# Performance work log

Hardware: AMD Instinct MI355X
Metric: run time of the kernel (lower is better)

Reference implementation:

```python
import jax, jax.numpy as jnp
import numpy as np

N = 100000   # nodes
E = 1200000  # edges
D = 64       # feature / hidden dim (heads=1)
L = 3        # num_layers
G = 64       # num graphs
SCALE = 1.0 / np.sqrt(D)


def setup_inputs() -> dict:
    key = jax.random.key(0)
    ks = jax.random.split(key, 12)
    inp = {
        "x": jax.random.normal(ks[0], (N, D), dtype=jnp.float32),
        "edge_index": jax.random.randint(ks[1], (2, E), 0, N, dtype=jnp.int64),
        "batch": jnp.sort(jax.random.randint(ks[2], (N,), 0, G, dtype=jnp.int64)),
        "Wq": jax.random.normal(ks[3], (L, D, D), dtype=jnp.float32) * 0.1,
        "bq": jax.random.normal(ks[4], (L, D), dtype=jnp.float32) * 0.1,
        "Wk": jax.random.normal(ks[5], (L, D, D), dtype=jnp.float32) * 0.1,
        "bk": jax.random.normal(ks[6], (L, D), dtype=jnp.float32) * 0.1,
        "Wv": jax.random.normal(ks[7], (L, D, D), dtype=jnp.float32) * 0.1,
        "bv": jax.random.normal(ks[8], (L, D), dtype=jnp.float32) * 0.1,
        "Ws": jax.random.normal(ks[9], (L, D, D), dtype=jnp.float32) * 0.1,
        "bs": jax.random.normal(ks[10], (L, D), dtype=jnp.float32) * 0.1,
    }
    return inp


def _transformer_conv(x, src, dst, Wq, bq, Wk, bk, Wv, bv, Ws, bs):
    # PyG TransformerConv, heads=1, concat=True, root_weight=True, beta=False
    q = x @ Wq + bq            # [N, D] query of target nodes
    k = x @ Wk + bk            # [N, D] key of source nodes
    v = x @ Wv + bv            # [N, D] value of source nodes
    logits = jnp.sum(q[dst] * k[src], axis=-1) * SCALE  # [E]
    # segment softmax over incoming edges of each target node
    m = jax.ops.segment_max(logits, dst, num_segments=N)        # [N]
    e = jnp.exp(logits - m[dst])                                 # [E]
    denom = jax.ops.segment_sum(e, dst, num_segments=N)         # [N]
    alpha = e / denom[dst]                                       # [E]
    agg = jax.ops.segment_sum(alpha[:, None] * v[src], dst, num_segments=N)  # [N, D]
    return agg + x @ Ws + bs   # root/skip connection


def reference(x, edge_index, batch, Wq, bq, Wk, bk, Wv, bv, Ws, bs):
    src, dst = edge_index[0], edge_index[1]
    for l in range(L):
        x = _transformer_conv(x, src, dst, Wq[l], bq[l], Wk[l], bk[l],
                              Wv[l], bv[l], Ws[l], bs[l])
        x = jax.nn.relu(x)
    # global_mean_pool
    sums = jax.ops.segment_sum(x, batch, num_segments=G)                  # [G, D]
    counts = jax.ops.segment_sum(jnp.ones((N,), x.dtype), batch, num_segments=G)
    graph_emb = sums / jnp.maximum(counts, 1.0)[:, None]
    return (x, graph_emb)
```

## Files before the change

### kernel.cpp

```cpp
#include <hip/hip_runtime.h>
#include <math.h>

#define DD 64
#define APAD 512

typedef _Float16 h2 __attribute__((ext_vector_type(2)));
typedef _Float16 h4 __attribute__((ext_vector_type(4)));
typedef _Float16 h8 __attribute__((ext_vector_type(8)));
typedef float f32x4 __attribute__((ext_vector_type(4)));

__global__ __launch_bounds__(256) void k_hist(
    const int* __restrict__ dst, int* __restrict__ deg,
    unsigned short* __restrict__ pos, int ecnt)
{
  int e = (blockIdx.x * 256 + threadIdx.x) * 4;
  if (e + 3 < ecnt) {
    int4 d = *(const int4*)(dst + e);
    ushort4 pv;
    pv.x = (unsigned short)atomicAdd(deg + d.x, 1);
    pv.y = (unsigned short)atomicAdd(deg + d.y, 1);
    pv.z = (unsigned short)atomicAdd(deg + d.z, 1);
    pv.w = (unsigned short)atomicAdd(deg + d.w, 1);
    *(ushort4*)(pos + e) = pv;
  } else {
    for (; e < ecnt; ++e)
      pos[e] = (unsigned short)atomicAdd(deg + dst[e], 1);
  }
}

__global__ __launch_bounds__(256) void k_mix(
    const float* __restrict__ Wq, const float* __restrict__ Wk,
    const float* __restrict__ Wv, const float* __restrict__ Ws,
    _Float16* __restrict__ wf,
    const float* __restrict__ x, _Float16* __restrict__ xb,
    const int* __restrict__ deg, int* __restrict__ rowptr,
    int* __restrict__ btot, int* __restrict__ dbins,
    int nbk, int wb, int total8, int n)
{
  int tid = threadIdx.x;
  int bid = blockIdx.x;
  if (bid < nbk) {
    __shared__ int wsum[4];
    __shared__ int lbin[256];
    int lane = tid & 63, wave = tid >> 6;
    lbin[tid] = 0;
    __syncthreads();
    int i = bid * 1024 + tid * 4;
    int4 d = make_int4(0, 0, 0, 0);
    if (i + 3 < n) d = *(const int4*)(deg + i);
    else {
      if (i     < n) d.x = deg[i];
      if (i + 1 < n) d.y = deg[i + 1];
      if (i + 2 < n) d.z = deg[i + 2];
    }
    if (i     < n) atomicAdd(&lbin[min(d.x, 255)], 1);
    if (i + 1 < n) atomicAdd(&lbin[min(d.y, 255)], 1);
    if (i + 2 < n) atomicAdd(&lbin[min(d.z, 255)], 1);
    if (i + 3 < n) atomicAdd(&lbin[min(d.w, 255)], 1);

    int s1 = d.x, s2 = s1 + d.y, s3 = s2 + d.z, s4 = s3 + d.w;
    int s = s4;
    #pragma unroll
    for (int off = 1; off < 64; off <<= 1) {
      int t = __shfl_up(s, off);
      if (lane >= off) s += t;
    }
    if (lane == 63) wsum[wave] = s;
    __syncthreads();
    if (wave == 0) {
      int ws = (lane < 4) ? wsum[lane] : 0;
      #pragma unroll
      for (int off = 1; off < 4; off <<= 1) {
        int t = __shfl_up(ws, off);
        if (lane >= off) ws += t;
      }
      if (lane < 4) wsum[lane] = ws;
    }
    __syncthreads();
    int excl = ((wave > 0) ? wsum[wave - 1] : 0) + s - s4;
    if (i     < n) rowptr[i + 1] = excl + s1;
    if (i + 1 < n) rowptr[i + 2] = excl + s2;
    if (i + 2 < n) rowptr[i + 3] = excl + s3;
    if (i + 3 < n) rowptr[i + 4] = excl + s4;
    if (tid == 0) {
      if (bid == 0) rowptr[0] = 0;
      btot[bid] = wsum[3];
    }
    if (lbin[tid]) atomicAdd(&dbins[tid], lbin[tid]);
  } else if (bid < nbk + wb) {
    int id = (bid - nbk) * 4 + (tid >> 6);
    int lane = tid & 63;
    int layer = id >> 5;
    int c = (id >> 1) & 15;
    int s = id & 1;
    int col = c * 16 + (lane & 15);
    int mi = col >> 6;
    const float* W = (mi == 0 ? Wq : mi == 1 ? Wk : mi == 2 ? Wv : Ws)
                     + (size_t)layer * DD * DD;
    int colw = col & 63;
    _Float16* o = wf + ((((size_t)(layer * 16 + c)) * 2 + s) * 64 + lane) * 8;
    #pragma unroll
    for (int j = 0; j < 8; ++j) {
      int k = s * 32 + (lane >> 4) * 8 + j;
      o[j] = (_Float16)W[k * DD + colw];
    }
  } else {
    int i = (bid - nbk - wb) * 256 + tid;
    if (i >= total8) return;
    float4 a = ((const float4*)x)[i * 2];
    float4 b = ((const float4*)x)[i * 2 + 1];
    h8 o;
    o[0] = (_Float16)a.x; o[1] = (_Float16)a.y; o[2] = (_Float16)a.z; o[3] = (_Float16)a.w;
    o[4] = (_Float16)b.x; o[5] = (_Float16)b.y; o[6] = (_Float16)b.z; o[7] = (_Float16)b.w;
    *(h8*)(xb + (size_t)i * 8) = o;
  }
}

__global__ __launch_bounds__(64) void k_scanB(
    int* __restrict__ btot, int nb, const int* __restrict__ dbins,
    int* __restrict__ dcur)
{
  int lane = threadIdx.x;
  int v0 = (lane < nb) ? btot[lane] : 0;
  int v1 = (64 + lane < nb) ? btot[64 + lane] : 0;
  int s0 = v0;
  #pragma unroll
  for (int off = 1; off < 64; off <<= 1) {
    int t = __shfl_up(s0, off);
    if (lane >= off) s0 += t;
  }
  int tot0 = __shfl(s0, 63);
  int s1 = v1;
  #pragma unroll
  for (int off = 1; off < 64; off <<= 1) {
    int t = __shfl_up(s1, off);
    if (lane >= off) s1 += t;
  }
  if (lane < nb) btot[lane] = s0 - v0;
  if (64 + lane < nb) btot[64 + lane] = tot0 + s1 - v1;

  int4 dv = *(const int4*)(dbins + lane * 4);
  int t1 = dv.x, t2 = t1 + dv.y, t3 = t2 + dv.z, t4 = t3 + dv.w;
  int ss = t4;
  #pragma unroll
  for (int off = 1; off < 64; off <<= 1) {
    int t = __shfl_up(ss, off);
    if (lane >= off) ss += t;
  }
  int ex = ss - t4;
  dcur[lane * 4]     = ex;
  dcur[lane * 4 + 1] = ex + t1;
  dcur[lane * 4 + 2] = ex + t2;
  dcur[lane * 4 + 3] = ex + t3;
}

__global__ __launch_bounds__(1024) void k_scanCD(
    int* __restrict__ rowptr, const int* __restrict__ btot,
    const int* __restrict__ deg, int* __restrict__ dcur,
    int* __restrict__ order, int n)
{
  __shared__ int lcnt[256];
  __shared__ int lbase[256];
  int tid = threadIdx.x;
  int b = blockIdx.x;
  int off = btot[b];
  int i = b * 1024 + tid;
  if (off && i < n) rowptr[i + 1] += off;
  if (tid < 256) lcnt[tid] = 0;
  __syncthreads();
  int bin = 0, slot = 0;
  bool ok = (i < n);
  if (ok) {
    bin = min(deg[i], 255);
    slot = atomicAdd(&lcnt[bin], 1);
  }
  __syncthreads();
  if (tid < 256 && lcnt[tid]) lbase[tid] = atomicAdd(&dcur[tid], lcnt[tid]);
  __syncthreads();
  if (ok) order[(n - 1) - (lbase[bin] + slot)] = i;
}

#define LH_STRIDE 200
#define LS_STRIDE 72
#define WAVE_LDS  (16 * 400 + 16 * 144)

__device__ __forceinline__ void projM_body(
    int blk, int tid, char* lds,
    const _Float16* __restrict__ xb, const _Float16* __restrict__ wf,
    const float* __restrict__ bq, const float* __restrict__ bk,
    const float* __restrict__ bv, const float* __restrict__ bs,
    _Float16* __restrict__ qh, _Float16* __restrict__ kvh,
    _Float16* __restrict__ sh, int n)
{
  int wave = tid >> 6;
  int lane = tid & 63;
  int nbase = blk * 64 + wave * 16;
  if (nbase >= n) return;

  char* wbase = lds + wave * WAVE_LDS;
  _Float16* lh = (_Float16*)wbase;
  _Float16* ls = (_Float16*)(wbase + 16 * 400);

  const int cl = lane & 15;
  const int rq = lane >> 4;

  int ar = min(nbase + cl, n - 1);
  h8 a0 = *(const h8*)(xb + (size_t)ar * DD + rq * 8);
  h8 a1 = *(const h8*)(xb + (size_t)ar * DD + 32 + rq * 8);

  #pragma unroll
  for (int c = 0; c < 16; ++c) {
    const float* bp = (c < 4) ? bq : (c < 8) ? bk : (c < 12) ? bv : bs;
    const int fb = c * 16 + rq * 4;
    float4 b4 = *(const float4*)(bp + (fb & 63));
    f32x4 acc; acc[0] = b4.x; acc[1] = b4.y; acc[2] = b4.z; acc[3] = b4.w;
    const _Float16* wp = wf + ((size_t)(c * 2) * 64 + lane) * 8;
    h8 w0 = *(const h8*)(wp);
    h8 w1 = *(const h8*)(wp + 64 * 8);
    acc = __builtin_amdgcn_mfma_f32_16x16x32_f16(w0, a0, acc, 0, 0, 0);
    acc = __builtin_amdgcn_mfma_f32_16x16x32_f16(w1, a1, acc, 0, 0, 0);

    h4 o; o[0] = (_Float16)acc[0]; o[1] = (_Float16)acc[1];
    o[2] = (_Float16)acc[2]; o[3] = (_Float16)acc[3];
    if (c < 12)
      *(h4*)(lh + cl * LH_STRIDE + fb) = o;
    else
      *(h4*)(ls + cl * LS_STRIDE + (fb - 192)) = o;
  }

  #pragma unroll
  for (int i = 0; i < 2; ++i) {
    int chunk = i * 64 + lane;
    int nd = chunk >> 3, co = chunk & 7;
    h8 v = *(const h8*)(lh + nd * LH_STRIDE + co * 8);
    if (nbase + nd < n)
      *(h8*)(qh + (size_t)(nbase + nd) * DD + co * 8) = v;
  }
  #pragma unroll
  for (int i = 0; i < 4; ++i) {
    int chunk = i * 64 + lane;
    int nd = chunk >> 4, co = chunk & 15;
    h8 v = *(const h8*)(lh + nd * LH_STRIDE + 64 + co * 8);
    if (nbase + nd < n)
      *(h8*)(kvh + (size_t)(nbase + nd) * 128 + co * 8) = v;
  }
  #pragma unroll
  for (int i = 0; i < 2; ++i) {
    int chunk = i * 64 + lane;
    int nd = chunk >> 3, co = chunk & 7;
    h8 v = *(const h8*)(ls + nd * LS_STRIDE + co * 8);
    if (nbase + nd < n)
      *(h8*)(sh + (size_t)(nbase + nd) * DD + co * 8) = v;
  }
}

__global__ __launch_bounds__(256) void k_projM(
    const _Float16* __restrict__ xb, const _Float16* __restrict__ wf,
    const float* __restrict__ bq, const float* __restrict__ bk,
    const float* __restrict__ bv, const float* __restrict__ bs,
    _Float16* __restrict__ qh, _Float16* __restrict__ kvh,
    _Float16* __restrict__ sh, int n)
{
  __shared__ __align__(16) char lds[4 * WAVE_LDS];
  projM_body(blockIdx.x, threadIdx.x, lds, xb, wf, bq, bk, bv, bs,
             qh, kvh, sh, n);
}

__global__ __launch_bounds__(256) void k_fillproj(
    const int* __restrict__ src, const int* __restrict__ dst,
    const int* __restrict__ rowptr, const unsigned short* __restrict__ pos,
    int* __restrict__ adj, int ecnt, int hbk,
    const _Float16* __restrict__ xb, const _Float16* __restrict__ wf,
    const float* __restrict__ bq, const float* __restrict__ bk,
    const float* __restrict__ bv, const float* __restrict__ bs,
    _Float16* __restrict__ qh, _Float16* __restrict__ kvh,
    _Float16* __restrict__ sh, int n)
{
  __shared__ __align__(16) char lds[4 * WAVE_LDS];
  int bid = blockIdx.x;
  if (bid < hbk) {
    int e = (bid * 256 + threadIdx.x) * 4;
    if (e + 3 < ecnt) {
      int4 d = *(const int4*)(dst + e);
      int4 s = *(const int4*)(src + e);
      ushort4 p = *(const ushort4*)(pos + e);
      adj[rowptr[d.x] + p.x] = s.x;
      adj[rowptr[d.y] + p.y] = s.y;
      adj[rowptr[d.z] + p.z] = s.z;
      adj[rowptr[d.w] + p.w] = s.w;
    } else {
      for (; e < ecnt; ++e)
        adj[rowptr[dst[e]] + pos[e]] = src[e];
    }
  } else {
    projM_body(bid - hbk, threadIdx.x, lds, xb, wf, bq, bk, bv, bs,
               qh, kvh, sh, n);
  }
}

#define H2OF(v, i) __builtin_shufflevector((v), (v), 2*(i), 2*(i)+1)

template<bool LAST>
__global__ __launch_bounds__(256) void k_node(
    const _Float16* __restrict__ qh, const _Float16* __restrict__ kvh,
    const int* __restrict__ rowptr, const int* __restrict__ adj,
    const int* __restrict__ order,
    const _Float16* __restrict__ sh, float* __restrict__ outp,
    _Float16* __restrict__ xbnext, int n)
{
  int wid = (blockIdx.x * blockDim.x + threadIdx.x) >> 6;
  int lane = threadIdx.x & 63;
  const int g = lane >> 3;
  const int t = lane & 7;

  int idx = wid * 8 + g;
  bool nok = (idx < n);
  int node = order[nok ? idx : (n - 1)];

  const h8 q8 = *(const h8*)(qh + (size_t)node * DD + t * 8);
  const h2 qp0 = H2OF(q8, 0), qp1 = H2OF(q8, 1), qp2 = H2OF(q8, 2), qp3 = H2OF(q8, 3);

  const int e0 = rowptr[node];
  const int d  = nok ? (rowptr[node + 1] - e0) : 0;

  float mg = -1e30f, den = 0.f;
  float agg[8] = {0.f, 0.f, 0.f, 0.f, 0.f, 0.f, 0.f, 0.f};

  const char* kvb = (const char*)kvh;
  const unsigned tb = (unsigned)t << 4;

  h8 kP, vP;
  {
    int s = adj[e0];
    unsigned off = ((unsigned)s << 8) + tb;
    kP = *(const h8*)(kvb + off);
    vP = *(const h8*)(kvb + off + 128);
  }

  for (int it = 0; it < d; ++it) {
    const h8 kc = kP, vc = vP;
    {
      int s2 = adj[e0 + it + 1];
      unsigned off = ((unsigned)s2 << 8) + tb;
      kP = *(const h8*)(kvb + off);
      vP = *(const h8*)(kvb + off + 128);
    }

#if __has_builtin(__builtin_amdgcn_fdot2)
    float p = __builtin_amdgcn_fdot2(qp0, H2OF(kc, 0), 0.f, false);
    p = __builtin_amdgcn_fdot2(qp1, H2OF(kc, 1), p, false);
    p = __builtin_amdgcn_fdot2(qp2, H2OF(kc, 2), p, false);
    p = __builtin_amdgcn_fdot2(qp3, H2OF(kc, 3), p, false);
#else
    h2 ph = qp0 * H2OF(kc, 0);
    ph = qp1 * H2OF(kc, 1) + ph;
    ph = qp2 * H2OF(kc, 2) + ph;
    ph = qp3 * H2OF(kc, 3) + ph;
    float p = (float)ph.x + (float)ph.y;
#endif
    p += __shfl_xor(p, 1);
    p += __shfl_xor(p, 2);
    p += __shfl_xor(p, 4);
    p *= 0.125f;

    if (p > mg) {
      float c = __expf(mg - p);
      den *= c;
      #pragma unroll
      for (int j = 0; j < 8; ++j) agg[j] *= c;
      mg = p;
    }
    float w = __expf(p - mg);
    den += w;
    #pragma unroll
    for (int j = 0; j < 8; ++j)
      agg[j] = fmaf(w, (float)vc[j], agg[j]);
  }

  if (nok) {
    float inv = (den > 0.f) ? (1.0f / den) : 0.f;
    const h8 s8 = *(const h8*)(sh + (size_t)node * DD + t * 8);
    float r[8];
    #pragma unroll
    for (int j = 0; j < 8; ++j)
      r[j] = fmaxf(fmaf(agg[j], inv, (float)s8[j]), 0.f);
    if (LAST) {
      float* op = outp + (size_t)node * DD + t * 8;
      *(float4*)(op)     = make_float4(r[0], r[1], r[2], r[3]);
      *(float4*)(op + 4) = make_float4(r[4], r[5], r[6], r[7]);
    } else {
      h8 xh;
      #pragma unroll
      for (int j = 0; j < 8; ++j) xh[j] = (_Float16)r[j];
      *(h8*)(xbnext + (size_t)node * DD + t * 8) = xh;
    }
  }
}

__global__ __launch_bounds__(64) void k_pool_sum(
    const float* __restrict__ x, const int* __restrict__ batch,
    float* __restrict__ gsum, int n)
{
  int lane = threadIdx.x;
  int n0 = blockIdx.x * 64;
  if (n0 >= n) return;
  int n1 = min(n0 + 64, n);
  float acc = 0.f;
  int g_prev = batch[n0];
  for (int nn = n0; nn < n1; ++nn) {
    int g = batch[nn];
    if (g != g_prev) {
      atomicAdd(gsum + (size_t)g_prev * DD + lane, acc);
      acc = 0.f; g_prev = g;
    }
    acc += x[(size_t)nn * DD + lane];
  }
  atomicAdd(gsum + (size_t)g_prev * DD + lane, acc);
}

__device__ __forceinline__ int lbound(const int* __restrict__ a, int n, int key)
{
  int lo = 0, hi = n;
  while (lo < hi) {
    int mid = (lo + hi) >> 1;
    if (a[mid] < key) lo = mid + 1; else hi = mid;
  }
  return lo;
}

__global__ __launch_bounds__(256) void k_pool_div(
    const float* __restrict__ gsum, const int* __restrict__ batch,
    float* __restrict__ emb, int gtot, int n)
{
  int gid = blockIdx.x * blockDim.x + threadIdx.x;
  if (gid >= gtot * DD) return;
  int g = gid >> 6;
  int cnt = lbound(batch, n, g + 1) - lbound(batch, n, g);
  emb[gid] = gsum[gid] / fmaxf((float)cnt, 1.0f);
}

extern "C" void kernel_launch(void* const* d_in, const int* in_sizes, int n_in,
                              void* d_out, int out_size, void* d_ws, size_t ws_size,
                              hipStream_t stream)
{
  const float* x_in  = (const float*)d_in[0];
  const int*   ei    = (const int*)  d_in[1];
  const int*   batch = (const int*)  d_in[2];
  const float* Wq = (const float*)d_in[3];
  const float* bq = (const float*)d_in[4];
  const float* Wk = (const float*)d_in[5];
  const float* bk = (const float*)d_in[6];
  const float* Wv = (const float*)d_in[7];
  const float* bv = (const float*)d_in[8];
  const float* Ws = (const float*)d_in[9];
  const float* bs = (const float*)d_in[10];

  const int nd     = in_sizes[0];
  const int n      = nd / DD;
  const int ecnt   = in_sizes[1] / 2;
  const int layers = in_sizes[3] / (DD * DD);
  const int gtot   = (out_size - nd) / DD;

  const int* src = ei;
  const int* dst = ei + ecnt;

  char* cur = (char*)d_ws;
  _Float16*  SH  = (_Float16*)cur;  cur += (size_t)nd * 2;
  _Float16*  XB  = (_Float16*)cur;  cur += (size_t)nd * 2;
  _Float16*  QH  = (_Float16*)cur;  cur += (size_t)nd * 2;
  _Float16*  KVH = (_Float16*)cur;  cur += (size_t)nd * 4;
  _Float16*  WF  = (_Float16*)cur;  cur += (size_t)layers * 16384 * 2;
  int* rowptr = (int*)cur;          cur += (size_t)(n + 4) * 4;
  int* adj    = (int*)cur;          cur += (size_t)(ecnt + APAD) * 4;
  int* deg    = (int*)cur;          cur += (size_t)n * 4;
  int* dbins  = (int*)cur;          cur += 256 * 4;
  float* gsum = (float*)cur;        cur += (size_t)gtot * DD * 4;
  int* dcur   = (int*)cur;          cur += 256 * 4;
  int* btot   = (int*)cur;          cur += 128 * 4;
  int* order  = (int*)cur;          cur += (size_t)n * 4;
  unsigned short* pos = (unsigned short*)cur; cur += (size_t)ecnt * 2;

  float* out = (float*)d_out;

  hipMemsetAsync(adj + ecnt, 0,
                 (size_t)(APAD + n + 256 + gtot * DD) * 4, stream);

  const int hbk = (ecnt + 1023) / 1024;
  const int nbk = (n + 1023) / 1024;
  const int wb  = layers * 8;
  const int xbk = (n * 8 + 255) / 256;
  const int pj  = (n + 63) / 64;
  const int nb  = (n + 31) / 32;

  k_hist<<<hbk, 256, 0, stream>>>(dst, deg, pos, ecnt);
  k_mix<<<nbk + wb + xbk, 256, 0, stream>>>(Wq, Wk, Wv, Ws, WF, x_in, XB,
                                            deg, rowptr, btot, dbins,
                                            nbk, wb, n * 8, n);
  k_scanB<<<1, 64, 0, stream>>>(btot, nbk, dbins, dcur);
  k_scanCD<<<nbk, 1024, 0, stream>>>(rowptr, btot, deg, dcur, order, n);

  k_fillproj<<<hbk + pj, 256, 0, stream>>>(src, dst, rowptr, pos, adj, ecnt,
                                           hbk, XB, WF, bq, bk, bv, bs,
                                           QH, KVH, SH, n);
  for (int l = 0; l < layers; ++l) {
    if (l > 0) {
      const size_t bo = (size_t)l * DD;
      k_projM<<<pj, 256, 0, stream>>>(XB, WF + (size_t)l * 16384,
                                      bq + bo, bk + bo, bv + bo, bs + bo,
                                      QH, KVH, SH, n);
    }
    if (l == layers - 1)
      k_node<true><<<nb, 256, 0, stream>>>(QH, KVH, rowptr, adj, order,
                                           SH, out, XB, n);
    else
      k_node<false><<<nb, 256, 0, stream>>>(QH, KVH, rowptr, adj, order,
                                            SH, out, XB, n);
  }

  const int pbk = (n + 63) / 64;
  k_pool_sum<<<pbk, 64, 0, stream>>>(out, batch, gsum, n);
  const int fb = (gtot * DD + 255) / 256;
  k_pool_div<<<fb, 256, 0, stream>>>(gsum, batch, out + (size_t)nd, gtot, n);
}
```

Before: 322.2 us.

## Fuse scan, degree-bin ordering, CSR fill and projection into one kernel

```diff
diff --git a/kernel.cpp b/kernel.cpp
--- a/kernel.cpp
+++ b/kernel.cpp
@@ -116,70 +116,6 @@
   }
 }
 
-__global__ __launch_bounds__(64) void k_scanB(
-    int* __restrict__ btot, int nb, const int* __restrict__ dbins,
-    int* __restrict__ dcur)
-{
-  int lane = threadIdx.x;
-  int v0 = (lane < nb) ? btot[lane] : 0;
-  int v1 = (64 + lane < nb) ? btot[64 + lane] : 0;
-  int s0 = v0;
-  #pragma unroll
-  for (int off = 1; off < 64; off <<= 1) {
-    int t = __shfl_up(s0, off);
-    if (lane >= off) s0 += t;
-  }
-  int tot0 = __shfl(s0, 63);
-  int s1 = v1;
-  #pragma unroll
-  for (int off = 1; off < 64; off <<= 1) {
-    int t = __shfl_up(s1, off);
-    if (lane >= off) s1 += t;
-  }
-  if (lane < nb) btot[lane] = s0 - v0;
-  if (64 + lane < nb) btot[64 + lane] = tot0 + s1 - v1;
-
-  int4 dv = *(const int4*)(dbins + lane * 4);
-  int t1 = dv.x, t2 = t1 + dv.y, t3 = t2 + dv.z, t4 = t3 + dv.w;
-  int ss = t4;
-  #pragma unroll
-  for (int off = 1; off < 64; off <<= 1) {
-    int t = __shfl_up(ss, off);
-    if (lane >= off) ss += t;
-  }
-  int ex = ss - t4;
-  dcur[lane * 4]     = ex;
-  dcur[lane * 4 + 1] = ex + t1;
-  dcur[lane * 4 + 2] = ex + t2;
-  dcur[lane * 4 + 3] = ex + t3;
-}
-
-__global__ __launch_bounds__(1024) void k_scanCD(
-    int* __restrict__ rowptr, const int* __restrict__ btot,
-    const int* __restrict__ deg, int* __restrict__ dcur,
-    int* __restrict__ order, int n)
-{
-  __shared__ int lcnt[256];
-  __shared__ int lbase[256];
-  int tid = threadIdx.x;
-  int b = blockIdx.x;
-  int off = btot[b];
-  int i = b * 1024 + tid;
-  if (off && i < n) rowptr[i + 1] += off;
-  if (tid < 256) lcnt[tid] = 0;
-  __syncthreads();
-  int bin = 0, slot = 0;
-  bool ok = (i < n);
-  if (ok) {
-    bin = min(deg[i], 255);
-    slot = atomicAdd(&lcnt[bin], 1);
-  }
-  __syncthreads();
-  if (tid < 256 && lcnt[tid]) lbase[tid] = atomicAdd(&dcur[tid], lcnt[tid]);
-  __syncthreads();
-  if (ok) order[(n - 1) - (lbase[bin] + slot)] = i;
-}
-
 #define LH_STRIDE 200
 #define LS_STRIDE 72
 #define WAVE_LDS  (16 * 400 + 16 * 144)
@@ -266,34 +202,115 @@
              qh, kvh, sh, n);
 }
 
-__global__ __launch_bounds__(256) void k_fillproj(
+__global__ __launch_bounds__(256) void k_build(
+    int* __restrict__ rowptr, const int* __restrict__ btot,
+    const int* __restrict__ deg, const int* __restrict__ dbins,
+    int* __restrict__ dcur2, int* __restrict__ rowfin,
+    int* __restrict__ order,
     const int* __restrict__ src, const int* __restrict__ dst,
-    const int* __restrict__ rowptr, const unsigned short* __restrict__ pos,
-    int* __restrict__ adj, int ecnt, int hbk,
+    const unsigned short* __restrict__ pos, int* __restrict__ adj,
     const _Float16* __restrict__ xb, const _Float16* __restrict__ wf,
     const float* __restrict__ bq, const float* __restrict__ bk,
     const float* __restrict__ bv, const float* __restrict__ bs,
     _Float16* __restrict__ qh, _Float16* __restrict__ kvh,
-    _Float16* __restrict__ sh, int n)
+    _Float16* __restrict__ sh,
+    int n, int ecnt, int nbk, int hbk)
 {
   __shared__ __align__(16) char lds[4 * WAVE_LDS];
+  int tid = threadIdx.x;
   int bid = blockIdx.x;
-  if (bid < hbk) {
-    int e = (bid * 256 + threadIdx.x) * 4;
+
+  if (bid < nbk) {
+    int* lcnt    = (int*)lds;
+    int* lbase   = lcnt + 256;
+    int* binbase = lbase + 256;
+    int* sh_off  = binbase + 256;
+    lcnt[tid] = 0;
+    int lane = tid & 63, wave = tid >> 6;
+    if (wave == 0) {
+      int acc = 0;
+      for (int j = lane; j < bid; j += 64) acc += btot[j];
+      #pragma unroll
+      for (int off = 1; off < 64; off <<= 1) acc += __shfl_xor(acc, off);
+      if (lane == 0) sh_off[0] = acc;
+    } else if (wave == 1) {
+      int4 dv = *(const int4*)(dbins + lane * 4);
+      int t1 = dv.x, t2 = t1 + dv.y, t3 = t2 + dv.z, t4 = t3 + dv.w;
+      int ss = t4;
+      #pragma unroll
+      for (int off = 1; off < 64; off <<= 1) {
+        int t = __shfl_up(ss, off);
+        if (lane >= off) ss += t;
+      }
+      int ex = ss - t4;
+      binbase[lane * 4]     = ex;
+      binbase[lane * 4 + 1] = ex + t1;
+      binbase[lane * 4 + 2] = ex + t2;
+      binbase[lane * 4 + 3] = ex + t3;
+    }
+    __syncthreads();
+    const int off_b = sh_off[0];
+    int i = bid * 1024 + tid * 4;
+    int bins[4], slots[4];
+    #pragma unroll
+    for (int k = 0; k < 4; ++k) {
+      int ii = i + k;
+      if (ii < n) {
+        rowfin[ii + 1] = rowptr[ii + 1] + off_b;
+        bins[k] = min(deg[ii], 255);
+        slots[k] = atomicAdd(&lcnt[bins[k]], 1);
+      }
+    }
+    __syncthreads();
+    if (lcnt[tid]) lbase[tid] = binbase[tid] + atomicAdd(&dcur2[tid], lcnt[tid]);
+    __syncthreads();
+    #pragma unroll
+    for (int k = 0; k < 4; ++k) {
+      int ii = i + k;
+      if (ii < n)
+        order[(n - 1) - (lbase[bins[k]] + slots[k])] = ii;
+    }
+    if (bid == 0 && tid == 0) rowfin[0] = 0;
+  } else if (bid < nbk + hbk) {
+    int* offarr = (int*)lds;
+    if (tid < 64) {
+      int lane = tid;
+      int v0 = (lane < nbk) ? btot[lane] : 0;
+      int v1 = (64 + lane < nbk) ? btot[64 + lane] : 0;
+      int s0 = v0;
+      #pragma unroll
+      for (int off = 1; off < 64; off <<= 1) {
+        int t = __shfl_up(s0, off);
+        if (lane >= off) s0 += t;
+      }
+      int tot0 = __shfl(s0, 63);
+      int s1 = v1;
+      #pragma unroll
+      for (int off = 1; off < 64; off <<= 1) {
+        int t = __shfl_up(s1, off);
+        if (lane >= off) s1 += t;
+      }
+      offarr[lane] = s0 - v0;
+      offarr[64 + lane] = tot0 + s1 - v1;
+    }
+    __syncthreads();
+    int e = ((bid - nbk) * 256 + tid) * 4;
     if (e + 3 < ecnt) {
       int4 d = *(const int4*)(dst + e);
       int4 s = *(const int4*)(src + e);
       ushort4 p = *(const ushort4*)(pos + e);
-      adj[rowptr[d.x] + p.x] = s.x;
-      adj[rowptr[d.y] + p.y] = s.y;
-      adj[rowptr[d.z] + p.z] = s.z;
-      adj[rowptr[d.w] + p.w] = s.w;
+      adj[rowptr[d.x] + offarr[max(d.x - 1, 0) >> 10] + p.x] = s.x;
+      adj[rowptr[d.y] + offarr[max(d.y - 1, 0) >> 10] + p.y] = s.y;
+      adj[rowptr[d.z] + offarr[max(d.z - 1, 0) >> 10] + p.z] = s.z;
+      adj[rowptr[d.w] + offarr[max(d.w - 1, 0) >> 10] + p.w] = s.w;
     } else {
-      for (; e < ecnt; ++e)
-        adj[rowptr[dst[e]] + pos[e]] = src[e];
+      for (; e < ecnt; ++e) {
+        int d = dst[e];
+        adj[rowptr[d] + offarr[max(d - 1, 0) >> 10] + pos[e]] = src[e];
+      }
     }
   } else {
-    projM_body(bid - hbk, threadIdx.x, lds, xb, wf, bq, bk, bv, bs,
+    projM_body(bid - nbk - hbk, tid, lds, xb, wf, bq, bk, bv, bs,
                qh, kvh, sh, n);
   }
 }
@@ -303,7 +320,7 @@
 template<bool LAST>
 __global__ __launch_bounds__(256) void k_node(
     const _Float16* __restrict__ qh, const _Float16* __restrict__ kvh,
-    const int* __restrict__ rowptr, const int* __restrict__ adj,
+    const int* __restrict__ rowfin, const int* __restrict__ adj,
     const int* __restrict__ order,
     const _Float16* __restrict__ sh, float* __restrict__ outp,
     _Float16* __restrict__ xbnext, int n)
@@ -320,8 +337,8 @@
   const h8 q8 = *(const h8*)(qh + (size_t)node * DD + t * 8);
   const h2 qp0 = H2OF(q8, 0), qp1 = H2OF(q8, 1), qp2 = H2OF(q8, 2), qp3 = H2OF(q8, 3);
 
-  const int e0 = rowptr[node];
-  const int d  = nok ? (rowptr[node + 1] - e0) : 0;
+  const int e0 = rowfin[node];
+  const int d  = nok ? (rowfin[node + 1] - e0) : 0;
 
   float mg = -1e30f, den = 0.f;
   float agg[8] = {0.f, 0.f, 0.f, 0.f, 0.f, 0.f, 0.f, 0.f};
@@ -471,11 +488,12 @@
   _Float16*  KVH = (_Float16*)cur;  cur += (size_t)nd * 4;
   _Float16*  WF  = (_Float16*)cur;  cur += (size_t)layers * 16384 * 2;
   int* rowptr = (int*)cur;          cur += (size_t)(n + 4) * 4;
+  int* rowfin = (int*)cur;          cur += (size_t)(n + 4) * 4;
   int* adj    = (int*)cur;          cur += (size_t)(ecnt + APAD) * 4;
   int* deg    = (int*)cur;          cur += (size_t)n * 4;
   int* dbins  = (int*)cur;          cur += 256 * 4;
+  int* dcur2  = (int*)cur;          cur += 256 * 4;
   float* gsum = (float*)cur;        cur += (size_t)gtot * DD * 4;
-  int* dcur   = (int*)cur;          cur += 256 * 4;
   int* btot   = (int*)cur;          cur += 128 * 4;
   int* order  = (int*)cur;          cur += (size_t)n * 4;
   unsigned short* pos = (unsigned short*)cur; cur += (size_t)ecnt * 2;
@@ -483,7 +501,7 @@
   float* out = (float*)d_out;
 
   hipMemsetAsync(adj + ecnt, 0,
-                 (size_t)(APAD + n + 256 + gtot * DD) * 4, stream);
+                 (size_t)(APAD + n + 512 + gtot * DD) * 4, stream);
 
   const int hbk = (ecnt + 1023) / 1024;
   const int nbk = (n + 1023) / 1024;
@@ -496,12 +514,13 @@
   k_mix<<<nbk + wb + xbk, 256, 0, stream>>>(Wq, Wk, Wv, Ws, WF, x_in, XB,
                                             deg, rowptr, btot, dbins,
                                             nbk, wb, n * 8, n);
-  k_scanB<<<1, 64, 0, stream>>>(btot, nbk, dbins, dcur);
-  k_scanCD<<<nbk, 1024, 0, stream>>>(rowptr, btot, deg, dcur, order, n);
-
-  k_fillproj<<<hbk + pj, 256, 0, stream>>>(src, dst, rowptr, pos, adj, ecnt,
-                                           hbk, XB, WF, bq, bk, bv, bs,
-                                           QH, KVH, SH, n);
+  k_build<<<nbk + hbk + pj, 256, 0, stream>>>(rowptr, btot, deg, dbins,
+                                              dcur2, rowfin, order,
+                                              src, dst, pos, adj,
+                                              XB, WF, bq, bk, bv, bs,
+                                              QH, KVH, SH,
+                                              n, ecnt, nbk, hbk);
+
   for (int l = 0; l < layers; ++l) {
     if (l > 0) {
       const size_t bo = (size_t)l * DD;
@@ -510,10 +529,10 @@
                                       QH, KVH, SH, n);
     }
     if (l == layers - 1)
-      k_node<true><<<nb, 256, 0, stream>>>(QH, KVH, rowptr, adj, order,
+      k_node<true><<<nb, 256, 0, stream>>>(QH, KVH, rowfin, adj, order,
                                            SH, out, XB, n);
     else
-      k_node<false><<<nb, 256, 0, stream>>>(QH, KVH, rowptr, adj, order,
+      k_node<false><<<nb, 256, 0, stream>>>(QH, KVH, rowfin, adj, order,
                                             SH, out, XB, n);
   }
 
```

After: 324.1 us. Within noise of the previous version (+0.6%).
